# Kernel optimization log

Measured on AMD Instinct MI355X. Metric: run time of the kernel, lower is better.

Reference implementation:

```python
import jax, jax.numpy as jnp
import numpy as np

DMODEL = 1024
DHIDDEN = 1024
N_HEAD = 16
HEAD_DIM = DHIDDEN // N_HEAD
B, S = 4, 2048


def setup_inputs() -> dict:
    key = jax.random.key(0)
    ks = jax.random.split(key, 10)
    sc = 1.0 / np.sqrt(DMODEL)
    return {
        "x": jax.random.normal(ks[0], (B, S, DMODEL), dtype=jnp.float32),
        "Wq": jax.random.normal(ks[1], (DMODEL, DHIDDEN), dtype=jnp.float32) * sc,
        "bq": jnp.zeros((DHIDDEN,), dtype=jnp.float32),
        "Wk": jax.random.normal(ks[2], (DMODEL, DHIDDEN), dtype=jnp.float32) * sc,
        "bk": jnp.zeros((DHIDDEN,), dtype=jnp.float32),
        "Wv": jax.random.normal(ks[3], (DMODEL, DHIDDEN), dtype=jnp.float32) * sc,
        "bv": jnp.zeros((DHIDDEN,), dtype=jnp.float32),
        "Wo": jax.random.normal(ks[4], (DHIDDEN, DMODEL), dtype=jnp.float32) * sc,
        "bo": jnp.zeros((DMODEL,), dtype=jnp.float32),
        "ln_gamma": jnp.ones((DMODEL,), dtype=jnp.float32),
        "ln_beta": jnp.zeros((DMODEL,), dtype=jnp.float32),
    }


def _layernorm(x, gamma, beta, eps=1e-5):
    mu = jnp.mean(x, axis=-1, keepdims=True)
    var = jnp.var(x, axis=-1, keepdims=True)
    return (x - mu) * jax.lax.rsqrt(var + eps) * gamma + beta


def reference(x, Wq, bq, Wk, bk, Wv, bv, Wo, bo, ln_gamma, ln_beta):
    b, s, _ = x.shape
    h = _layernorm(x, ln_gamma, ln_beta)           # [B,S,D]
    q = h @ Wq + bq                                 # [B,S,Dh]
    k = h @ Wk + bk
    v = h @ Wv + bv
    # [B,H,S,hd]
    q = q.reshape(b, s, N_HEAD, HEAD_DIM).transpose(0, 2, 1, 3)
    k = k.reshape(b, s, N_HEAD, HEAD_DIM).transpose(0, 2, 1, 3)
    v = v.reshape(b, s, N_HEAD, HEAD_DIM).transpose(0, 2, 1, 3)
    scores = jnp.einsum("bhqd,bhkd->bhqk", q, k) / np.sqrt(HEAD_DIM)
    causal = jnp.tril(jnp.ones((s, s), dtype=bool))  # [S,S]
    scores = jnp.where(causal, scores, jnp.finfo(scores.dtype).min)
    attn = jax.nn.softmax(scores, axis=-1)           # [B,H,S,S]
    out = jnp.einsum("bhqk,bhkd->bhqd", attn, v)     # [B,H,S,hd]
    out = out.transpose(0, 2, 1, 3).reshape(b, s, DHIDDEN)
    return out @ Wo + bo
```

## Files before the change

### kernel.cpp

```cpp
#include <hip/hip_runtime.h>


typedef short short8 __attribute__((ext_vector_type(8)));
typedef float floatx4 __attribute__((ext_vector_type(4)));
typedef unsigned short ushort4v __attribute__((ext_vector_type(4)));
typedef unsigned int uint2v __attribute__((ext_vector_type(2)));

#define MFMA16(a, b, c) __builtin_amdgcn_mfma_f32_16x16x32_bf16((a), (b), (c), 0, 0, 0)

__device__ __forceinline__ unsigned short f2bf(float f) {
  unsigned int u = __float_as_uint(f);
  u += 0x7FFFu + ((u >> 16) & 1u);
  return (unsigned short)(u >> 16);
}

#if defined(__has_builtin)
#if __has_builtin(__builtin_amdgcn_cvt_pk_bf16_f32)
#define HAVE_PK_BF16 1
#endif
#if __has_builtin(__builtin_amdgcn_exp2f)
#define EXP2(x) __builtin_amdgcn_exp2f(x)
#endif
#if __has_builtin(__builtin_amdgcn_rcpf)
#define RCP(x) __builtin_amdgcn_rcpf(x)
#endif
#endif
#ifndef EXP2
#define EXP2(x) exp2f(x)
#endif
#ifndef RCP
#define RCP(x) (1.0f / (x))
#endif

__device__ __forceinline__ unsigned int pk_bf16(float a, float b) {
#ifdef HAVE_PK_BF16
  typedef __bf16 bf16x2_t __attribute__((ext_vector_type(2)));
  union { bf16x2_t v; unsigned int u; } cvt;
  cvt.v = __builtin_amdgcn_cvt_pk_bf16_f32(a, b);
  return cvt.u;
#else
  return (unsigned int)f2bf(a) | ((unsigned int)f2bf(b) << 16);
#endif
}

__device__ __forceinline__ void async_lds16(const void* g, void* l) {
  __builtin_amdgcn_global_load_lds(
      (const __attribute__((address_space(1))) void*)g,
      (__attribute__((address_space(3))) void*)l, 16, 0, 0);
}

__global__ __launch_bounds__(256) void prep_kernel(
    const float* __restrict__ wq, const float* __restrict__ wk,
    const float* __restrict__ wv, const float* __restrict__ wo,
    unsigned short* __restrict__ wqkvT, unsigned short* __restrict__ woT,
    const float* __restrict__ x, const float* __restrict__ gamma,
    const float* __restrict__ beta, unsigned short* __restrict__ h) {
  __shared__ float t[64][65];
  __shared__ float sm[4], qm[4];
  const int id = (int)blockIdx.x;
  const int tid = threadIdx.x;
  if (id < 1024) {
    const int mz = id >> 8, rem = id & 255;
    const int n0 = (rem & 15) * 64, k0 = (rem >> 4) * 64;
    const int r = tid >> 6, c = tid & 63;
    const float* src = (mz == 0) ? wq : (mz == 1) ? wk : (mz == 2) ? wv : wo;
    unsigned short* dst = (mz == 3) ? woT : (wqkvT + (size_t)mz * 1024 * 1024);
#pragma unroll
    for (int i = r; i < 64; i += 4) t[i][c] = src[(size_t)(k0 + i) * 1024 + n0 + c];
    __syncthreads();
#pragma unroll
    for (int i = r; i < 64; i += 4)
      dst[(size_t)(n0 + i) * 1024 + k0 + c] = f2bf(t[c][i]);
    return;
  }
  const int row = id - 1024;
  const float4 xv = ((const float4*)(x + (size_t)row * 1024))[tid];
  float s = xv.x + xv.y + xv.z + xv.w;
  float q = xv.x * xv.x + xv.y * xv.y + xv.z * xv.z + xv.w * xv.w;
#pragma unroll
  for (int off = 32; off > 0; off >>= 1) {
    s += __shfl_xor(s, off, 64);
    q += __shfl_xor(q, off, 64);
  }
  const int wave = tid >> 6, lane = tid & 63;
  if (lane == 0) { sm[wave] = s; qm[wave] = q; }
  __syncthreads();
  s = sm[0] + sm[1] + sm[2] + sm[3];
  q = qm[0] + qm[1] + qm[2] + qm[3];
  const float mean = s * (1.0f / 1024.0f);
  const float var = q * (1.0f / 1024.0f) - mean * mean;
  const float rstd = rsqrtf(var + 1e-5f);
  const float4 g = ((const float4*)gamma)[tid];
  const float4 bb = ((const float4*)beta)[tid];
  ushort4v o;
  o.x = f2bf((xv.x - mean) * rstd * g.x + bb.x);
  o.y = f2bf((xv.y - mean) * rstd * g.y + bb.y);
  o.z = f2bf((xv.z - mean) * rstd * g.z + bb.z);
  o.w = f2bf((xv.w - mean) * rstd * g.w + bb.w);
  ((ushort4v*)(h + (size_t)row * 1024))[tid] = o;
}

#define GEMM128_MAIN(A_, Bt_, m0_, n0_)                                         \
  __shared__ __align__(16) unsigned short lAB[2][128 * 64];                     \
  unsigned short* const lA = &lAB[0][0];                                        \
  unsigned short* const lB = &lAB[1][0];                                        \
  const int tid = threadIdx.x;                                                  \
  const int wave = tid >> 6, lane = tid & 63, quad = lane >> 4, l15 = lane & 15;\
  const int wm = wave >> 1, wn = wave & 1;                                      \
  const int m0 = (m0_), n0 = (n0_);                                             \
  const int srow = tid >> 3, schunk = tid & 7;                                  \
  const int swz = l15 & 7;                                                      \
  floatx4 acc[4][4];                                                            \
  _Pragma("unroll") for (int i = 0; i < 4; i++)                                 \
  _Pragma("unroll") for (int j = 0; j < 4; j++)                                 \
      acc[i][j] = (floatx4){0.f, 0.f, 0.f, 0.f};                                \
  for (int kt = 0; kt < 16; kt++) {                                             \
    const int k0 = kt * 64;                                                     \
    __syncthreads();                                                            \
    _Pragma("unroll") for (int j = 0; j < 4; j++) {                             \
      const int row_ = j * 32 + srow;                                           \
      const int gch_ = schunk ^ (row_ & 7);                                     \
      async_lds16(A_ + (size_t)(m0 + row_) * 1024 + k0 + gch_ * 8,              \
                  (char*)lA + j * 4096 + wave * 1024);                          \
      async_lds16(Bt_ + (size_t)(n0 + row_) * 1024 + k0 + gch_ * 8,             \
                  (char*)lB + j * 4096 + wave * 1024);                          \
    }                                                                           \
    __syncthreads();                                                            \
    _Pragma("unroll") for (int kk = 0; kk < 2; kk++) {                          \
      const int ch = (kk * 4 + quad) ^ swz;                                     \
      short8 af[4], bf[4];                                                      \
      _Pragma("unroll") for (int i = 0; i < 4; i++) {                           \
        af[i] = *(const short8*)(lA + (wm * 64 + i * 16 + l15) * 64 + ch * 8);  \
        bf[i] = *(const short8*)(lB + (wn * 64 + i * 16 + l15) * 64 + ch * 8);  \
      }                                                                         \
      _Pragma("unroll") for (int mt = 0; mt < 4; mt++)                          \
      _Pragma("unroll") for (int nt = 0; nt < 4; nt++)                          \
          acc[mt][nt] = MFMA16(af[mt], bf[nt], acc[mt][nt]);                    \
    }                                                                           \
  }

__global__ __launch_bounds__(256) void gemm_qkv(
    const unsigned short* __restrict__ A, const unsigned short* __restrict__ Bt,
    const float* __restrict__ bq, const float* __restrict__ bk,
    const float* __restrict__ bv, unsigned short* __restrict__ qo,
    unsigned short* __restrict__ ko, unsigned short* __restrict__ vT) {
  const int id = (int)blockIdx.x;
  const int xcd = id & 7, rr = id >> 3;
  GEMM128_MAIN(A, Bt, (xcd * 8 + (rr & 7)) * 128, (rr >> 3) * 128)
  const int sel = n0 >> 10;
  const float* bias = (sel == 0) ? bq : (sel == 1) ? bk : bv;
  const float oscale = (sel == 0) ? 0.18033688011112042f : 1.0f;
  unsigned short* const st = &lAB[0][0];
  const int b16 = (m0 >> 11) * 16;
  const int h0 = (n0 & 1023) >> 6;
  const int ms = m0 & 2047;
  __syncthreads();
  if (sel == 2) {
#pragma unroll
    for (int nt = 0; nt < 4; nt++) {
      const int nl = wn * 64 + nt * 16 + l15;
      const float bia = bias[(n0 + nl) & 1023];
      const int x = (nl & 15) << 1;
#pragma unroll
      for (int mt = 0; mt < 4; mt++) {
        const int chunk = wm * 16 + mt * 4 + quad;
        ushort4v pk;
#pragma unroll
        for (int r = 0; r < 4; r++) pk[r] = f2bf(acc[mt][nt][r] + bia);
        *(ushort4v*)((char*)st + nl * 256 + ((chunk ^ x) << 3)) = pk;
      }
    }
    __syncthreads();
#pragma unroll
    for (int p = 0; p < 8; p++) {
      const int nl = p * 16 + (tid >> 4);
      const int j2 = tid & 15;
      const short8 vv =
          *(const short8*)((char*)st + nl * 256 + ((j2 ^ (nl & 15)) << 4));
      *(short8*)(vT + ((size_t)(b16 + h0 + (nl >> 6)) * 64 + (nl & 63)) * 2048 +
                 ms + j2 * 8) = vv;
    }
  } else {
#pragma unroll
    for (int nt = 0; nt < 4; nt++) {
      const int nl = wn * 64 + nt * 16 + l15;
      const float bia = bias[(n0 + nl) & 1023];
      const int chunk = nl >> 3, nin = nl & 7;
#pragma unroll
      for (int mt = 0; mt < 4; mt++) {
#pragma unroll
        for (int r = 0; r < 4; r++) {
          const int ml = wm * 64 + mt * 16 + quad * 4 + r;
          *(unsigned short*)((char*)st + ml * 256 + ((chunk ^ (ml & 7)) << 4) +
                             nin * 2) = f2bf((acc[mt][nt][r] + bia) * oscale);
        }
      }
    }
    __syncthreads();
    unsigned short* const dq = (sel == 0) ? qo : ko;
#pragma unroll
    for (int p = 0; p < 8; p++) {
      const int ml = p * 16 + (tid >> 4);
      const int j = tid & 15;
      const short8 vv =
          *(const short8*)((char*)st + ml * 256 + ((j ^ (ml & 7)) << 4));
      *(short8*)(dq + ((size_t)(b16 + h0 + (j >> 3)) * 2048 + (ms + ml)) * 64 +
                 (j & 7) * 8) = vv;
    }
  }
}

__global__ __launch_bounds__(256) void gemm_out(
    const unsigned short* __restrict__ A, const unsigned short* __restrict__ Bt,
    const float* __restrict__ bo, float* __restrict__ out) {
  __shared__ __align__(16) unsigned short lA[64 * 64];
  __shared__ __align__(16) unsigned short lB[128 * 64];
  const int tid = threadIdx.x;
  const int wave = tid >> 6, lane = tid & 63, quad = lane >> 4, l15 = lane & 15;
  const int id = (int)blockIdx.x;
  const int xcd = id & 7, rr = id >> 3;
  const int m0 = (xcd * 16 + (rr & 15)) * 64;
  const int n0 = (rr >> 4) * 128;
  const int srow = tid >> 3, schunk = tid & 7;
  const int swz = l15 & 7;
  floatx4 acc[4][2];
#pragma unroll
  for (int i = 0; i < 4; i++)
#pragma unroll
    for (int j = 0; j < 2; j++) acc[i][j] = (floatx4){0.f, 0.f, 0.f, 0.f};
  for (int kt = 0; kt < 16; kt++) {
    const int k0 = kt * 64;
    __syncthreads();
#pragma unroll
    for (int j = 0; j < 2; j++) {
      const int row_ = j * 32 + srow;
      const int gch_ = schunk ^ (row_ & 7);
      async_lds16(A + (size_t)(m0 + row_) * 1024 + k0 + gch_ * 8,
                  (char*)lA + j * 4096 + wave * 1024);
    }
#pragma unroll
    for (int j = 0; j < 4; j++) {
      const int row_ = j * 32 + srow;
      const int gch_ = schunk ^ (row_ & 7);
      async_lds16(Bt + (size_t)(n0 + row_) * 1024 + k0 + gch_ * 8,
                  (char*)lB + j * 4096 + wave * 1024);
    }
    __syncthreads();
#pragma unroll
    for (int kk = 0; kk < 2; kk++) {
      const int ch = (kk * 4 + quad) ^ swz;
      short8 af[4], bf[2];
#pragma unroll
      for (int i = 0; i < 4; i++)
        af[i] = *(const short8*)(lA + (i * 16 + l15) * 64 + ch * 8);
#pragma unroll
      for (int i = 0; i < 2; i++)
        bf[i] = *(const short8*)(lB + (wave * 32 + i * 16 + l15) * 64 + ch * 8);
#pragma unroll
      for (int mt = 0; mt < 4; mt++)
#pragma unroll
        for (int nt = 0; nt < 2; nt++)
          acc[mt][nt] = MFMA16(af[mt], bf[nt], acc[mt][nt]);
    }
  }
#pragma unroll
  for (int nt = 0; nt < 2; nt++) {
    const int n = n0 + wave * 32 + nt * 16 + l15;
    const float bia = bo[n];
#pragma unroll
    for (int mt = 0; mt < 4; mt++) {
      const int m = m0 + mt * 16 + quad * 4;
#pragma unroll
      for (int r = 0; r < 4; r++) out[(size_t)(m + r) * 1024 + n] = acc[mt][nt][r] + bia;
    }
  }
}

__global__ __launch_bounds__(256, 4) void attn_kernel(
    const unsigned short* __restrict__ q, const unsigned short* __restrict__ k,
    const unsigned short* __restrict__ vT, unsigned short* __restrict__ ao) {
  __shared__ __align__(16) unsigned short lK[2][64 * 64];
  __shared__ __align__(16) unsigned short lV[2][64 * 64];
  __shared__ __align__(16) unsigned short lP[4][16 * 64];
  const int tid = threadIdx.x;
  const int wave = tid >> 6, lane = tid & 63, quad = lane >> 4, l15 = lane & 15;
  const int id = (int)blockIdx.x;
  const int bh = (id & 7) * 8 + ((id >> 3) & 7);
  const int qx = id >> 6;
  const int b = bh >> 4, hh = bh & 15;
  const int qtA = 31 - qx, qtB = qx;
  const int q0wA = qtA * 64 + wave * 16, q0wB = qtB * 64 + wave * 16;
  const int ntiles = qtA + 1;

  const unsigned short* qb = q + (size_t)bh * 2048 * 64;
  const unsigned short* kb = k + (size_t)bh * 2048 * 64;
  const unsigned short* vb = vT + (size_t)bh * 64 * 2048;
  unsigned short* pw = &lP[wave][0];

  const int srow = tid >> 3, schunk = tid & 7;

  const short8 ones8 = {0x3F80, 0x3F80, 0x3F80, 0x3F80,
                        0x3F80, 0x3F80, 0x3F80, 0x3F80};

  const int sw = l15 & 7;
  const int ph0 = (0 * 4 + quad) ^ sw, ph1 = (1 * 4 + quad) ^ sw;

#define STAGE_TILE(src_, rstride_, cbase_, dst_)                                 \
  _Pragma("unroll") for (int j = 0; j < 2; j++) {                                \
    const int row_ = j * 32 + srow;                                              \
    const int gch_ = schunk ^ (row_ & 7);                                        \
    async_lds16(src_ + (size_t)row_ * (rstride_) + (cbase_) + gch_ * 8,          \
                (char*)(dst_) + j * 4096 + wave * 1024);                         \
  }

  short8 qfA[2], qfB[2];
#pragma unroll
  for (int hf = 0; hf < 2; hf++) {
    qfA[hf] = *(const short8*)(qb + (size_t)(q0wA + l15) * 64 + hf * 32 + quad * 8);
    qfB[hf] = *(const short8*)(qb + (size_t)(q0wB + l15) * 64 + hf * 32 + quad * 8);
  }

  floatx4 oA[4], oB[4];
#pragma unroll
  for (int nt = 0; nt < 4; nt++) {
    oA[nt] = (floatx4){0.f, 0.f, 0.f, 0.f};
    oB[nt] = (floatx4){0.f, 0.f, 0.f, 0.f};
  }
  floatx4 laccA = {0.f, 0.f, 0.f, 0.f}, laccB = {0.f, 0.f, 0.f, 0.f};

  STAGE_TILE(kb, 64, 0, &lK[0][0])
  STAGE_TILE(vb, 2048, 0, &lV[0][0])
  int kbase = 0;
  for (int t = 0; t < ntiles; t++, kbase += 64) {
    __syncthreads();
    if (t + 1 < ntiles) {
      const int nb = (t + 1) & 1;
      STAGE_TILE(kb, 64, (size_t)(kbase + 64) * 64, &lK[nb][0])
      STAGE_TILE(vb, 2048, (size_t)(kbase + 64), &lV[nb][0])
    }
    const unsigned short* lKc = &lK[t & 1][0];
    const unsigned short* lVc = &lV[t & 1][0];
    const bool dual = (t <= qtB);

    floatx4 scA[4], scB[4];
    __builtin_amdgcn_s_setprio(1);
#pragma unroll
    for (int nt = 0; nt < 4; nt++) {
      scA[nt] = (floatx4){0.f, 0.f, 0.f, 0.f};
      scB[nt] = (floatx4){0.f, 0.f, 0.f, 0.f};
      const short8 kf0 = *(const short8*)(lKc + (nt * 16 + l15) * 64 + ph0 * 8);
      const short8 kf1 = *(const short8*)(lKc + (nt * 16 + l15) * 64 + ph1 * 8);
      scA[nt] = MFMA16(kf0, qfA[0], scA[nt]);
      scA[nt] = MFMA16(kf1, qfA[1], scA[nt]);
      if (dual) {
        scB[nt] = MFMA16(kf0, qfB[0], scB[nt]);
        scB[nt] = MFMA16(kf1, qfB[1], scB[nt]);
      }
    }
    __builtin_amdgcn_s_setprio(0);

    {
      const bool needmask = (kbase + 63 > q0wA);
      const int qg = q0wA + l15;
#pragma unroll
      for (int nt = 0; nt < 4; nt++) {
        float p0 = EXP2(scA[nt][0]), p1 = EXP2(scA[nt][1]);
        float p2 = EXP2(scA[nt][2]), p3 = EXP2(scA[nt][3]);
        if (needmask) {
          const int kk = kbase + nt * 16 + quad * 4;
          if (kk + 0 > qg) p0 = 0.f;
          if (kk + 1 > qg) p1 = 0.f;
          if (kk + 2 > qg) p2 = 0.f;
          if (kk + 3 > qg) p3 = 0.f;
        }
        uint2v pk2;
        pk2.x = pk_bf16(p0, p1);
        pk2.y = pk_bf16(p2, p3);
        const int phys = (nt * 2 + (quad >> 1)) ^ sw;
        *(uint2v*)(pw + l15 * 64 + phys * 8 + (quad & 1) * 4) = pk2;
      }
    }
    asm volatile("s_waitcnt lgkmcnt(0)" ::: "memory");
    short8 pfA0 = *(const short8*)(pw + l15 * 64 + ph0 * 8);
    short8 pfA1 = *(const short8*)(pw + l15 * 64 + ph1 * 8);

    short8 pfB0, pfB1;
    if (dual) {
      const bool needmask = (kbase + 63 > q0wB);
      const int qg = q0wB + l15;
#pragma unroll
      for (int nt = 0; nt < 4; nt++) {
        float p0 = EXP2(scB[nt][0]), p1 = EXP2(scB[nt][1]);
        float p2 = EXP2(scB[nt][2]), p3 = EXP2(scB[nt][3]);
        if (needmask) {
          const int kk = kbase + nt * 16 + quad * 4;
          if (kk + 0 > qg) p0 = 0.f;
          if (kk + 1 > qg) p1 = 0.f;
          if (kk + 2 > qg) p2 = 0.f;
          if (kk + 3 > qg) p3 = 0.f;
        }
        uint2v pk2;
        pk2.x = pk_bf16(p0, p1);
        pk2.y = pk_bf16(p2, p3);
        const int phys = (nt * 2 + (quad >> 1)) ^ sw;
        *(uint2v*)(pw + l15 * 64 + phys * 8 + (quad & 1) * 4) = pk2;
      }
      asm volatile("s_waitcnt lgkmcnt(0)" ::: "memory");
      pfB0 = *(const short8*)(pw + l15 * 64 + ph0 * 8);
      pfB1 = *(const short8*)(pw + l15 * 64 + ph1 * 8);
    }

    __builtin_amdgcn_s_setprio(1);
#pragma unroll
    for (int hf = 0; hf < 2; hf++) {
      const short8 pfA = hf ? pfA1 : pfA0;
      laccA = MFMA16(ones8, pfA, laccA);
      if (dual) laccB = MFMA16(ones8, hf ? pfB1 : pfB0, laccB);
      const int ph = hf ? ph1 : ph0;
#pragma unroll
      for (int nt = 0; nt < 4; nt++) {
        const short8 vf = *(const short8*)(lVc + (nt * 16 + l15) * 64 + ph * 8);
        oA[nt] = MFMA16(vf, pfA, oA[nt]);
        if (dual) oB[nt] = MFMA16(vf, hf ? pfB1 : pfB0, oB[nt]);
      }
    }
    __builtin_amdgcn_s_setprio(0);
  }

  {
    const float linv = RCP(laccA[0]);
    unsigned short* dst = ao + ((size_t)b * 2048 + q0wA + l15) * 1024 + hh * 64;
#pragma unroll
    for (int nt = 0; nt < 4; nt++) {
      uint2v pk2;
      pk2.x = pk_bf16(oA[nt][0] * linv, oA[nt][1] * linv);
      pk2.y = pk_bf16(oA[nt][2] * linv, oA[nt][3] * linv);
      *(uint2v*)(dst + nt * 16 + quad * 4) = pk2;
    }
  }
  {
    const float linv = RCP(laccB[0]);
    unsigned short* dst = ao + ((size_t)b * 2048 + q0wB + l15) * 1024 + hh * 64;
#pragma unroll
    for (int nt = 0; nt < 4; nt++) {
      uint2v pk2;
      pk2.x = pk_bf16(oB[nt][0] * linv, oB[nt][1] * linv);
      pk2.y = pk_bf16(oB[nt][2] * linv, oB[nt][3] * linv);
      *(uint2v*)(dst + nt * 16 + quad * 4) = pk2;
    }
  }
#undef STAGE_TILE
}

extern "C" void kernel_launch(void* const* d_in, const int* in_sizes, int n_in,
                              void* d_out, int out_size, void* d_ws, size_t ws_size,
                              hipStream_t stream) {
  const float* x = (const float*)d_in[0];
  const float* Wq = (const float*)d_in[1];
  const float* bq = (const float*)d_in[2];
  const float* Wk = (const float*)d_in[3];
  const float* bk = (const float*)d_in[4];
  const float* Wv = (const float*)d_in[5];
  const float* bv = (const float*)d_in[6];
  const float* Wo = (const float*)d_in[7];
  const float* bo = (const float*)d_in[8];
  const float* gamma = (const float*)d_in[9];
  const float* beta = (const float*)d_in[10];
  float* out = (float*)d_out;

  char* ws = (char*)d_ws;
  unsigned short* wqkvT = (unsigned short*)(ws + 0);
  unsigned short* woT   = (unsigned short*)(ws + 6291456);
  unsigned short* h     = (unsigned short*)(ws + 8388608);
  unsigned short* qb    = (unsigned short*)(ws + 25165824);
  unsigned short* kb    = (unsigned short*)(ws + 41943040);
  unsigned short* vT    = (unsigned short*)(ws + 58720256);
  unsigned short* ao    = (unsigned short*)(ws + 75497472);

  hipLaunchKernelGGL(prep_kernel, dim3(9216), dim3(256), 0, stream,
                     Wq, Wk, Wv, Wo, wqkvT, woT, x, gamma, beta, h);
  hipLaunchKernelGGL(gemm_qkv, dim3(1536), dim3(256), 0, stream,
                     h, wqkvT, bq, bk, bv, qb, kb, vT);
  hipLaunchKernelGGL(attn_kernel, dim3(1024), dim3(256), 0, stream, qb, kb, vT, ao);
  hipLaunchKernelGGL(gemm_out, dim3(1024), dim3(256), 0, stream, ao, woT, bo, out);
}
```

Measured before the change: 270.7 us.

## Double-buffer QKV GEMM LDS tiles with K=32 stages to overlap loads

Replaces the single-buffered 64-wide K tile loop in the QKV projection GEMM with a double-buffered 32-wide K tile loop. The next stage's async global-to-LDS copies are issued before the MFMAs on the current stage, so load latency can hide behind compute, and only one barrier per iteration remains. The swizzle is adapted to the 32-element rows. This doubles the iteration count and halves the MFMA work between barriers. The async copies are not explicitly waited on before the barrier, so correctness relies on the barrier draining them.

New measurement: 287.9 us. 6.4% more time.

```diff
diff --git a/kernel.cpp b/kernel.cpp
--- a/kernel.cpp
+++ b/kernel.cpp
@@ -100,61 +100,70 @@
   ((ushort4v*)(h + (size_t)row * 1024))[tid] = o;
 }
 
-#define GEMM128_MAIN(A_, Bt_, m0_, n0_)                                         \
-  __shared__ __align__(16) unsigned short lAB[2][128 * 64];                     \
-  unsigned short* const lA = &lAB[0][0];                                        \
-  unsigned short* const lB = &lAB[1][0];                                        \
-  const int tid = threadIdx.x;                                                  \
-  const int wave = tid >> 6, lane = tid & 63, quad = lane >> 4, l15 = lane & 15;\
-  const int wm = wave >> 1, wn = wave & 1;                                      \
-  const int m0 = (m0_), n0 = (n0_);                                             \
-  const int srow = tid >> 3, schunk = tid & 7;                                  \
-  const int swz = l15 & 7;                                                      \
-  floatx4 acc[4][4];                                                            \
-  _Pragma("unroll") for (int i = 0; i < 4; i++)                                 \
-  _Pragma("unroll") for (int j = 0; j < 4; j++)                                 \
-      acc[i][j] = (floatx4){0.f, 0.f, 0.f, 0.f};                                \
-  for (int kt = 0; kt < 16; kt++) {                                             \
-    const int k0 = kt * 64;                                                     \
-    __syncthreads();                                                            \
-    _Pragma("unroll") for (int j = 0; j < 4; j++) {                             \
-      const int row_ = j * 32 + srow;                                           \
-      const int gch_ = schunk ^ (row_ & 7);                                     \
-      async_lds16(A_ + (size_t)(m0 + row_) * 1024 + k0 + gch_ * 8,              \
-                  (char*)lA + j * 4096 + wave * 1024);                          \
-      async_lds16(Bt_ + (size_t)(n0 + row_) * 1024 + k0 + gch_ * 8,             \
-                  (char*)lB + j * 4096 + wave * 1024);                          \
-    }                                                                           \
-    __syncthreads();                                                            \
-    _Pragma("unroll") for (int kk = 0; kk < 2; kk++) {                          \
-      const int ch = (kk * 4 + quad) ^ swz;                                     \
-      short8 af[4], bf[4];                                                      \
-      _Pragma("unroll") for (int i = 0; i < 4; i++) {                           \
-        af[i] = *(const short8*)(lA + (wm * 64 + i * 16 + l15) * 64 + ch * 8);  \
-        bf[i] = *(const short8*)(lB + (wn * 64 + i * 16 + l15) * 64 + ch * 8);  \
-      }                                                                         \
-      _Pragma("unroll") for (int mt = 0; mt < 4; mt++)                          \
-      _Pragma("unroll") for (int nt = 0; nt < 4; nt++)                          \
-          acc[mt][nt] = MFMA16(af[mt], bf[nt], acc[mt][nt]);                    \
-    }                                                                           \
-  }
-
 __global__ __launch_bounds__(256) void gemm_qkv(
     const unsigned short* __restrict__ A, const unsigned short* __restrict__ Bt,
     const float* __restrict__ bq, const float* __restrict__ bk,
     const float* __restrict__ bv, unsigned short* __restrict__ qo,
     unsigned short* __restrict__ ko, unsigned short* __restrict__ vT) {
+  __shared__ __align__(16) unsigned short lAB[2][2][128 * 32];
+  const int tid = threadIdx.x;
+  const int wave = tid >> 6, lane = tid & 63, quad = lane >> 4, l15 = lane & 15;
+  const int wm = wave >> 1, wn = wave & 1;
   const int id = (int)blockIdx.x;
   const int xcd = id & 7, rr = id >> 3;
-  GEMM128_MAIN(A, Bt, (xcd * 8 + (rr & 7)) * 128, (rr >> 3) * 128)
+  const int m0 = (xcd * 8 + (rr & 7)) * 128;
+  const int n0 = (rr >> 3) * 128;
+  const int srow4 = tid >> 2, schunk4 = tid & 3;
+  const int gchsw = schunk4 ^ ((srow4 & 3) ^ ((srow4 >> 2) & 3));
+  const int ch32 = ((quad ^ ((l15 & 3) ^ ((l15 >> 2) & 3)))) * 8;
+
+  floatx4 acc[4][4];
+#pragma unroll
+  for (int i = 0; i < 4; i++)
+#pragma unroll
+    for (int j = 0; j < 4; j++) acc[i][j] = (floatx4){0.f, 0.f, 0.f, 0.f};
+
+#define STG32(Mat_, base_, k0_, dst_)                                          \
+  _Pragma("unroll") for (int j_ = 0; j_ < 2; j_++) {                           \
+    async_lds16((Mat_) + (size_t)((base_) + j_ * 64 + srow4) * 1024 + (k0_) +  \
+                    gchsw * 8,                                                 \
+                (char*)(dst_) + j_ * 4096 + wave * 1024);                      \
+  }
+
+  STG32(A, m0, 0, &lAB[0][0][0]);
+  STG32(Bt, n0, 0, &lAB[1][0][0]);
+  __syncthreads();
+  for (int kt = 0; kt < 32; kt++) {
+    const int cur = kt & 1;
+    if (kt + 1 < 32) {
+      const int nxt = cur ^ 1;
+      STG32(A, m0, (kt + 1) * 32, &lAB[0][nxt][0]);
+      STG32(Bt, n0, (kt + 1) * 32, &lAB[1][nxt][0]);
+    }
+    const unsigned short* lAc = &lAB[0][cur][0];
+    const unsigned short* lBc = &lAB[1][cur][0];
+    short8 af[4], bf[4];
+#pragma unroll
+    for (int i = 0; i < 4; i++) {
+      af[i] = *(const short8*)(lAc + (wm * 64 + i * 16 + l15) * 32 + ch32);
+      bf[i] = *(const short8*)(lBc + (wn * 64 + i * 16 + l15) * 32 + ch32);
+    }
+#pragma unroll
+    for (int mt = 0; mt < 4; mt++)
+#pragma unroll
+      for (int nt = 0; nt < 4; nt++)
+        acc[mt][nt] = MFMA16(af[mt], bf[nt], acc[mt][nt]);
+    __syncthreads();
+  }
+#undef STG32
+
   const int sel = n0 >> 10;
   const float* bias = (sel == 0) ? bq : (sel == 1) ? bk : bv;
   const float oscale = (sel == 0) ? 0.18033688011112042f : 1.0f;
-  unsigned short* const st = &lAB[0][0];
+  unsigned short* const st = &lAB[0][0][0];
   const int b16 = (m0 >> 11) * 16;
   const int h0 = (n0 & 1023) >> 6;
   const int ms = m0 & 2047;
-  __syncthreads();
   if (sel == 2) {
 #pragma unroll
     for (int nt = 0; nt < 4; nt++) {
```
